# Optimization experiments

Hardware: AMD Instinct MI355X
Metric: run time of the kernel (lower is better)

Reference implementation:

```python
import jax, jax.numpy as jnp
import numpy as np

B, H, W, C = 64, 56, 56, 256
WS, SHIFT, HEADS = 7, 3, 8
N = WS * WS
HID = 4 * C


def _rel_pos_index():
    coords = np.stack(np.meshgrid(np.arange(WS), np.arange(WS), indexing='ij'))  # (2,ws,ws)
    flat = coords.reshape(2, -1)
    rel = (flat[:, :, None] - flat[:, None, :]).transpose(1, 2, 0)  # (N,N,2)
    rel[..., 0] += WS - 1
    rel[..., 1] += WS - 1
    rel[..., 0] *= 2 * WS - 1
    return rel.sum(-1)  # (N,N)


def _attn_mask():
    img = np.zeros((H, W), dtype=np.int32)
    cnt = 0
    for hs in (slice(0, -WS), slice(-WS, -SHIFT), slice(-SHIFT, None)):
        for ws_ in (slice(0, -WS), slice(-WS, -SHIFT), slice(-SHIFT, None)):
            img[hs, ws_] = cnt
            cnt += 1
    mw = img.reshape(H // WS, WS, W // WS, WS).transpose(0, 2, 1, 3).reshape(-1, N)  # (nW,N)
    diff = mw[:, None, :] - mw[:, :, None]
    return np.where(diff != 0, -100.0, 0.0).astype(np.float32)  # (nW,N,N)


def setup_inputs() -> dict:
    key = jax.random.key(0)
    ks = jax.random.split(key, 16)
    s = 0.02
    return {
        'x': jax.random.normal(ks[0], (B, H * W, C), jnp.float32),
        'norm1_g': jnp.ones((C,), jnp.float32),
        'norm1_b': jnp.zeros((C,), jnp.float32),
        'qkv_w': jax.random.normal(ks[1], (3 * C, C), jnp.float32) * s,
        'qkv_b': jnp.zeros((3 * C,), jnp.float32),
        'rpb_table': jax.random.normal(ks[2], ((2 * WS - 1) ** 2, HEADS), jnp.float32) * s,
        'proj_w': jax.random.normal(ks[3], (C, C), jnp.float32) * s,
        'proj_b': jnp.zeros((C,), jnp.float32),
        'norm2_g': jnp.ones((C,), jnp.float32),
        'norm2_b': jnp.zeros((C,), jnp.float32),
        'fc1_w': jax.random.normal(ks[4], (HID, C), jnp.float32) * s,
        'fc1_b': jnp.zeros((HID,), jnp.float32),
        'fc2_w': jax.random.normal(ks[5], (C, HID), jnp.float32) * s,
        'fc2_b': jnp.zeros((C,), jnp.float32),
        'rel_index': jnp.asarray(_rel_pos_index(), jnp.int32),
        'attn_mask': jnp.asarray(_attn_mask(), jnp.float32),
    }


def _ln(y, g, b):
    m = y.mean(-1, keepdims=True)
    v = ((y - m) ** 2).mean(-1, keepdims=True)
    return (y - m) / jnp.sqrt(v + 1e-5) * g + b


def reference(x, norm1_g, norm1_b, qkv_w, qkv_b, rpb_table, proj_w, proj_b,
              norm2_g, norm2_b, fc1_w, fc1_b, fc2_w, fc2_b, rel_index, attn_mask):
    Bx, L, Cx = x.shape
    shortcut = x
    y = _ln(x, norm1_g, norm1_b).reshape(Bx, H, W, Cx)
    # cyclic shift (roll_index_select equivalent)
    y = jnp.roll(y, (-SHIFT, -SHIFT), axis=(1, 2))
    # window partition -> (B*nW, N, C)
    y = y.reshape(Bx, H // WS, WS, W // WS, WS, Cx).transpose(0, 1, 3, 2, 4, 5).reshape(-1, N, Cx)
    B_ = y.shape[0]
    hd = Cx // HEADS
    qkv = (y @ qkv_w.T + qkv_b).reshape(B_, N, 3, HEADS, hd).transpose(2, 0, 3, 1, 4)
    q, k, v = qkv[0], qkv[1], qkv[2]
    scale = hd ** -0.5
    attn = jnp.einsum('bhnd,bhmd->bhnm', q * scale, k)  # (B_,H,N,N)
    rpb = rpb_table[rel_index.reshape(-1)].reshape(N, N, HEADS).transpose(2, 0, 1)
    attn = attn + rpb[None]
    nW = attn_mask.shape[0]
    attn = attn.reshape(B_ // nW, nW, HEADS, N, N) + attn_mask[None, :, None]
    attn = jax.nn.softmax(attn.reshape(B_, HEADS, N, N), axis=-1)
    o = jnp.einsum('bhnm,bhmd->bhnd', attn, v).transpose(0, 2, 1, 3).reshape(B_, N, Cx)
    o = o @ proj_w.T + proj_b
    # window reverse + reverse shift
    o = o.reshape(Bx, H // WS, W // WS, WS, WS, Cx).transpose(0, 1, 3, 2, 4, 5).reshape(Bx, H, W, Cx)
    o = jnp.roll(o, (SHIFT, SHIFT), axis=(1, 2)).reshape(Bx, L, Cx)
    x = shortcut + o  # drop_path prob = 0 / eval mode
    h = _ln(x, norm2_g, norm2_b)
    h = h @ fc1_w.T + fc1_b
    h = h * jax.nn.sigmoid(1.702 * h)  # fast_gelu
    h = h @ fc2_w.T + fc2_b
    return x + h
```

## Files before the change

kernel.cpp:

```cpp
#include <hip/hip_runtime.h>

typedef unsigned short u16;
typedef __attribute__((ext_vector_type(8))) short bf16x8;
typedef __attribute__((ext_vector_type(4))) float f32x4;

struct __align__(8) U16x4 { u16 x, y, z, w; };

__device__ __forceinline__ u16 f2bf(float f) {
  unsigned u = __float_as_uint(f);
  u = (u + 0x7FFFu + ((u >> 16) & 1u)) >> 16;
  return (u16)u;
}

__device__ __forceinline__ void gload16(const u16* g, u16* l) {
  __builtin_amdgcn_global_load_lds((const __attribute__((address_space(1))) void*)g,
                                   (__attribute__((address_space(3))) void*)l, 16, 0, 0);
}

#define MTOK 200704
#define CDIM 256
#define NC3  768
#define HIDD 1024

#define OFF_QKV   0UL
#define OFF_O     308281344UL
#define OFF_H1    0UL
#define OFF_Y     411041792UL
#define OFF_WQ    513802240UL
#define OFF_WP    514195456UL
#define OFF_W1    514326528UL
#define OFF_W2    514850816UL
#define OFF_RPB   515375104UL

__global__ __launch_bounds__(256) void prep_kernel(
    const float* __restrict__ qkv_w, const float* __restrict__ proj_w,
    const float* __restrict__ fc1_w, const float* __restrict__ fc2_w,
    const float* __restrict__ rpb_table, const int* __restrict__ rel_index,
    u16* wq, u16* wp, u16* w1, u16* w2, float* rpbf) {
  int i = blockIdx.x * 256 + threadIdx.x;
  if (i < 196608) { wq[i] = f2bf(qkv_w[i]); return; }
  int j = i - 196608;
  if (j < 65536) { wp[j] = f2bf(proj_w[j]); return; }
  int k = j - 65536;
  if (k < 262144) { w1[k] = f2bf(fc1_w[k]); return; }
  int l = k - 262144;
  if (l < 262144) { w2[l] = f2bf(fc2_w[l]); return; }
  int r = l - 262144;
  if (r < 8 * 2401) {
    int h = r / 2401, nm = r % 2401;
    rpbf[r] = rpb_table[rel_index[nm] * 8 + h];
  }
}

__global__ __launch_bounds__(256) void ln1_kernel(const float* __restrict__ x,
                                                  const float* __restrict__ gg,
                                                  const float* __restrict__ bb,
                                                  u16* __restrict__ y) {
  int wid = threadIdx.x >> 6, lane = threadIdx.x & 63;
  int m = blockIdx.x * 4 + wid;
  int win = m / 49, n = m % 49;
  int b = win >> 6, widx = win & 63;
  int hh = (widx >> 3) * 7 + n / 7 + 3; if (hh >= 56) hh -= 56;
  int ww = (widx & 7) * 7 + n % 7 + 3; if (ww >= 56) ww -= 56;
  const float* src = x + ((size_t)b * 3136 + hh * 56 + ww) * CDIM + lane * 4;
  float4 v = *(const float4*)src;
  float s = v.x + v.y + v.z + v.w;
  float s2 = v.x * v.x + v.y * v.y + v.z * v.z + v.w * v.w;
  for (int o = 32; o; o >>= 1) { s += __shfl_xor(s, o); s2 += __shfl_xor(s2, o); }
  float mean = s * (1.f / 256.f);
  float inv = rsqrtf(s2 * (1.f / 256.f) - mean * mean + 1e-5f);
  int c = lane * 4;
  float4 gv = *(const float4*)(gg + c);
  float4 bv = *(const float4*)(bb + c);
  U16x4 o4;
  o4.x = f2bf((v.x - mean) * inv * gv.x + bv.x);
  o4.y = f2bf((v.y - mean) * inv * gv.y + bv.y);
  o4.z = f2bf((v.z - mean) * inv * gv.z + bv.z);
  o4.w = f2bf((v.w - mean) * inv * gv.w + bv.w);
  *(U16x4*)(y + (size_t)m * CDIM + c) = o4;
}

__global__ __launch_bounds__(256) void ln2_kernel(const float* __restrict__ x2,
                                                  const float* __restrict__ gg,
                                                  const float* __restrict__ bb,
                                                  u16* __restrict__ y) {
  int wid = threadIdx.x >> 6, lane = threadIdx.x & 63;
  int m = blockIdx.x * 4 + wid;
  const float* src = x2 + (size_t)m * CDIM + lane * 4;
  float4 v = *(const float4*)src;
  float s = v.x + v.y + v.z + v.w;
  float s2 = v.x * v.x + v.y * v.y + v.z * v.z + v.w * v.w;
  for (int o = 32; o; o >>= 1) { s += __shfl_xor(s, o); s2 += __shfl_xor(s2, o); }
  float mean = s * (1.f / 256.f);
  float inv = rsqrtf(s2 * (1.f / 256.f) - mean * mean + 1e-5f);
  int c = lane * 4;
  float4 gv = *(const float4*)(gg + c);
  float4 bv = *(const float4*)(bb + c);
  U16x4 o4;
  o4.x = f2bf((v.x - mean) * inv * gv.x + bv.x);
  o4.y = f2bf((v.y - mean) * inv * gv.y + bv.y);
  o4.z = f2bf((v.z - mean) * inv * gv.z + bv.z);
  o4.w = f2bf((v.w - mean) * inv * gv.w + bv.w);
  *(U16x4*)(y + (size_t)m * CDIM + c) = o4;
}

template <int K>
__device__ __forceinline__ void gemm_tile(const u16* __restrict__ A, const u16* __restrict__ B,
                                          int m0, int n0, f32x4 acc[4][4], u16* lds) {
  const int tid = threadIdx.x;
  const int lane = tid & 63;
  const int lr = lane & 15, g = lane >> 4;
  const int wr = (tid >> 6) >> 1, wc = (tid >> 6) & 1;
  const int srow = tid >> 2;
  const int schunk = (tid & 3) ^ ((tid >> 3) & 3);
  const u16* ga = A + (size_t)(m0 + srow) * K + schunk * 8;
  const u16* gb = B + (size_t)(n0 + srow) * K + schunk * 8;
  const int swz = (g ^ ((lr >> 1) & 3)) * 8;

  auto STAGE = [&](int bsel, int k0) {
    u16* la = lds + bsel * 8192 + tid * 8;
    gload16(ga + k0, la);
    gload16(ga + (size_t)64 * K + k0, la + 2048);
    gload16(gb + k0, la + 4096);
    gload16(gb + (size_t)64 * K + k0, la + 6144);
  };
  auto COMPUTE = [&](int bsel) {
    const u16* ba = lds + bsel * 8192;
    const u16* bb = ba + 4096;
    bf16x8 af[4], bfr[4];
#pragma unroll
    for (int i = 0; i < 4; ++i) {
      af[i]  = *(const bf16x8*)(ba + (wr * 64 + i * 16 + lr) * 32 + swz);
      bfr[i] = *(const bf16x8*)(bb + (wc * 64 + i * 16 + lr) * 32 + swz);
    }
#pragma unroll
    for (int i = 0; i < 4; ++i)
#pragma unroll
      for (int j = 0; j < 4; ++j)
        acc[i][j] = __builtin_amdgcn_mfma_f32_16x16x32_bf16(bfr[j], af[i], acc[i][j], 0, 0, 0);
  };

  constexpr int NT = K / 32;
  STAGE(0, 0);
  __syncthreads();
  for (int t = 0; t < NT; t += 2) {
    if (t + 1 < NT) STAGE(1, (t + 1) * 32);
    COMPUTE(0);
    __syncthreads();
    if (t + 2 < NT) STAGE(0, (t + 2) * 32);
    COMPUTE(1);
    __syncthreads();
  }
}

__device__ __forceinline__ int xcd_swz(int bid, int nwg) {
  return (bid & 7) * (nwg >> 3) + (bid >> 3);
}

#define GEMM_PROLOG(NVAL, KVAL)                                            \
  __shared__ u16 lds[16384];                                               \
  const int NTX = (NVAL) / 128;                                            \
  int logical = xcd_swz(blockIdx.x, NTX * (MTOK / 128));                   \
  int m0 = (logical / NTX) * 128, n0 = (logical % NTX) * 128;              \
  f32x4 zero = {0.f, 0.f, 0.f, 0.f};                                       \
  f32x4 acc[4][4] = {{zero, zero, zero, zero}, {zero, zero, zero, zero},   \
                     {zero, zero, zero, zero}, {zero, zero, zero, zero}};  \
  gemm_tile<KVAL>(A, B, m0, n0, acc, lds);                                 \
  const int lane = threadIdx.x & 63;                                       \
  const int lr = lane & 15, g = lane >> 4;                                 \
  const int wid = threadIdx.x >> 6, wr = wid >> 1, wc = wid & 1;

__global__ __launch_bounds__(256) void gemm_qkv(const u16* __restrict__ A, const u16* __restrict__ B,
                                                const float* __restrict__ bias, u16* __restrict__ out) {
  GEMM_PROLOG(NC3, 256)
#pragma unroll
  for (int i = 0; i < 4; ++i) {
    int row = m0 + wr * 64 + i * 16 + lr;
#pragma unroll
    for (int j = 0; j < 4; ++j) {
      int cb = n0 + wc * 64 + j * 16 + g * 4;
      U16x4 o4;
      o4.x = f2bf(acc[i][j][0] + bias[cb + 0]);
      o4.y = f2bf(acc[i][j][1] + bias[cb + 1]);
      o4.z = f2bf(acc[i][j][2] + bias[cb + 2]);
      o4.w = f2bf(acc[i][j][3] + bias[cb + 3]);
      *(U16x4*)(out + (size_t)row * NC3 + cb) = o4;
    }
  }
}

__global__ __launch_bounds__(256) void gemm_proj(const u16* __restrict__ A, const u16* __restrict__ B,
                                                 const float* __restrict__ bias,
                                                 const float* __restrict__ x, float* __restrict__ x2) {
  GEMM_PROLOG(CDIM, 256)
#pragma unroll
  for (int i = 0; i < 4; ++i) {
    int row = m0 + wr * 64 + i * 16 + lr;
    int win = row / 49, n = row % 49;
    int b = win >> 6, widx = win & 63;
    int hh = (widx >> 3) * 7 + n / 7 + 3; if (hh >= 56) hh -= 56;
    int ww = (widx & 7) * 7 + n % 7 + 3; if (ww >= 56) ww -= 56;
    size_t dst = ((size_t)b * 3136 + hh * 56 + ww) * CDIM;
#pragma unroll
    for (int j = 0; j < 4; ++j) {
      int cb = n0 + wc * 64 + j * 16 + g * 4;
      float4 xv = *(const float4*)(x + dst + cb);
      float4 bv = *(const float4*)(bias + cb);
      float4 o4;
      o4.x = xv.x + acc[i][j][0] + bv.x;
      o4.y = xv.y + acc[i][j][1] + bv.y;
      o4.z = xv.z + acc[i][j][2] + bv.z;
      o4.w = xv.w + acc[i][j][3] + bv.w;
      *(float4*)(x2 + dst + cb) = o4;
    }
  }
}

__global__ __launch_bounds__(256) void gemm_fc1(const u16* __restrict__ A, const u16* __restrict__ B,
                                                const float* __restrict__ bias, u16* __restrict__ out) {
  GEMM_PROLOG(HIDD, 256)
#pragma unroll
  for (int i = 0; i < 4; ++i) {
    int row = m0 + wr * 64 + i * 16 + lr;
#pragma unroll
    for (int j = 0; j < 4; ++j) {
      int cb = n0 + wc * 64 + j * 16 + g * 4;
      float4 bv = *(const float4*)(bias + cb);
      float v0 = acc[i][j][0] + bv.x, v1 = acc[i][j][1] + bv.y;
      float v2 = acc[i][j][2] + bv.z, v3 = acc[i][j][3] + bv.w;
      v0 = v0 / (1.f + __expf(-1.702f * v0));
      v1 = v1 / (1.f + __expf(-1.702f * v1));
      v2 = v2 / (1.f + __expf(-1.702f * v2));
      v3 = v3 / (1.f + __expf(-1.702f * v3));
      U16x4 o4 = {f2bf(v0), f2bf(v1), f2bf(v2), f2bf(v3)};
      *(U16x4*)(out + (size_t)row * HIDD + cb) = o4;
    }
  }
}

__global__ __launch_bounds__(256) void gemm_fc2(const u16* __restrict__ A, const u16* __restrict__ B,
                                                const float* __restrict__ bias, float* __restrict__ out) {
  GEMM_PROLOG(CDIM, 1024)
#pragma unroll
  for (int i = 0; i < 4; ++i) {
    int row = m0 + wr * 64 + i * 16 + lr;
#pragma unroll
    for (int j = 0; j < 4; ++j) {
      int cb = n0 + wc * 64 + j * 16 + g * 4;
      float* p = out + (size_t)row * CDIM + cb;
      float4 ov = *(const float4*)p;
      float4 bv = *(const float4*)(bias + cb);
      ov.x += acc[i][j][0] + bv.x;
      ov.y += acc[i][j][1] + bv.y;
      ov.z += acc[i][j][2] + bv.z;
      ov.w += acc[i][j][3] + bv.w;
      *(float4*)p = ov;
    }
  }
}

__global__ __launch_bounds__(256) void attn_kernel(const u16* __restrict__ qkv,
                                                   const float* __restrict__ rpbf,
                                                   const float* __restrict__ mask,
                                                   u16* __restrict__ o) {
  __shared__ u16 p_lds[4][64][72];
  const int lane = threadIdx.x & 63, wid = threadIdx.x >> 6;
  const int lr = lane & 15, g = lane >> 4;
  const int win = blockIdx.x >> 1;
  const int head = (blockIdx.x & 1) * 4 + wid;
  const int widx = win & 63;
  const size_t base = (size_t)win * 49 * NC3 + head * 32;

  bf16x8 aq[4], bk[4];
#pragma unroll
  for (int R = 0; R < 4; ++R) {
    int n = R * 16 + lr; if (n > 48) n = 48;
    aq[R] = *(const bf16x8*)(qkv + base + (size_t)n * NC3 + 8 * g);
  }
#pragma unroll
  for (int Cc = 0; Cc < 4; ++Cc) {
    int mi = Cc * 16 + lr; if (mi > 48) mi = 48;
    bk[Cc] = *(const bf16x8*)(qkv + base + 256 + (size_t)mi * NC3 + 8 * g);
  }
  f32x4 zero = {0.f, 0.f, 0.f, 0.f};
  f32x4 s[4][4] = {{zero, zero, zero, zero}, {zero, zero, zero, zero},
                   {zero, zero, zero, zero}, {zero, zero, zero, zero}};
#pragma unroll
  for (int R = 0; R < 4; ++R)
#pragma unroll
    for (int Cc = 0; Cc < 4; ++Cc)
      s[R][Cc] = __builtin_amdgcn_mfma_f32_16x16x32_bf16(bk[Cc], aq[R], s[R][Cc], 0, 0, 0);

  const float scale = 0.17677669529663687f;
  const float* rpb_h = rpbf + head * 2401;
  const float* msk = mask + widx * 2401;
#pragma unroll
  for (int R = 0; R < 4; ++R) {
    int n = R * 16 + lr;
    bool nok = n < 49;
    int rbase = n * 49;
    float mx = -1e30f;
#pragma unroll
    for (int Cc = 0; Cc < 4; ++Cc)
#pragma unroll
      for (int reg = 0; reg < 4; ++reg) {
        int mc = Cc * 16 + g * 4 + reg;
        float v = (nok && mc < 49)
                    ? s[R][Cc][reg] * scale + rpb_h[rbase + mc] + msk[rbase + mc]
                    : -1e30f;
        s[R][Cc][reg] = v;
        mx = fmaxf(mx, v);
      }
    mx = fmaxf(mx, __shfl_xor(mx, 16));
    mx = fmaxf(mx, __shfl_xor(mx, 32));
    float sum = 0.f;
#pragma unroll
    for (int Cc = 0; Cc < 4; ++Cc)
#pragma unroll
      for (int reg = 0; reg < 4; ++reg) {
        float p = __expf(s[R][Cc][reg] - mx);
        s[R][Cc][reg] = p;
        sum += p;
      }
    sum += __shfl_xor(sum, 16);
    sum += __shfl_xor(sum, 32);
    float rs = 1.f / sum;
    int rowi = R * 16 + lr;
#pragma unroll
    for (int Cc = 0; Cc < 4; ++Cc) {
      U16x4 p4 = {f2bf(s[R][Cc][0] * rs), f2bf(s[R][Cc][1] * rs),
                  f2bf(s[R][Cc][2] * rs), f2bf(s[R][Cc][3] * rs)};
      *(U16x4*)(&p_lds[wid][rowi][Cc * 16 + g * 4]) = p4;
    }
  }
  __syncthreads();

  f32x4 oacc[4][2] = {{zero, zero}, {zero, zero}, {zero, zero}, {zero, zero}};
  const u16* vbase = qkv + base + 512;
#pragma unroll
  for (int ks = 0; ks < 2; ++ks) {
    bf16x8 bv[2];
#pragma unroll
    for (int D = 0; D < 2; ++D) {
#pragma unroll
      for (int i = 0; i < 8; ++i) {
        int mi = ks * 32 + 8 * g + i; if (mi > 48) mi = 48;
        bv[D][i] = (short)vbase[(size_t)mi * NC3 + D * 16 + lr];
      }
    }
#pragma unroll
    for (int R = 0; R < 4; ++R) {
      bf16x8 ap = *(const bf16x8*)(&p_lds[wid][R * 16 + lr][ks * 32 + 8 * g]);
      oacc[R][0] = __builtin_amdgcn_mfma_f32_16x16x32_bf16(bv[0], ap, oacc[R][0], 0, 0, 0);
      oacc[R][1] = __builtin_amdgcn_mfma_f32_16x16x32_bf16(bv[1], ap, oacc[R][1], 0, 0, 0);
    }
  }
#pragma unroll
  for (int R = 0; R < 4; ++R) {
    int n = R * 16 + lr;
    if (n < 49) {
#pragma unroll
      for (int D = 0; D < 2; ++D) {
        U16x4 o4 = {f2bf(oacc[R][D][0]), f2bf(oacc[R][D][1]),
                    f2bf(oacc[R][D][2]), f2bf(oacc[R][D][3])};
        *(U16x4*)(o + ((size_t)win * 49 + n) * CDIM + head * 32 + D * 16 + g * 4) = o4;
      }
    }
  }
}

extern "C" void kernel_launch(void* const* d_in, const int* in_sizes, int n_in,
                              void* d_out, int out_size, void* d_ws, size_t ws_size,
                              hipStream_t stream) {
  const float* x      = (const float*)d_in[0];
  const float* n1g    = (const float*)d_in[1];
  const float* n1b    = (const float*)d_in[2];
  const float* qkv_w  = (const float*)d_in[3];
  const float* qkv_b  = (const float*)d_in[4];
  const float* rpb_t  = (const float*)d_in[5];
  const float* proj_w = (const float*)d_in[6];
  const float* proj_b = (const float*)d_in[7];
  const float* n2g    = (const float*)d_in[8];
  const float* n2b    = (const float*)d_in[9];
  const float* fc1_w  = (const float*)d_in[10];
  const float* fc1_b  = (const float*)d_in[11];
  const float* fc2_w  = (const float*)d_in[12];
  const float* fc2_b  = (const float*)d_in[13];
  const int*   relidx = (const int*)d_in[14];
  const float* amask  = (const float*)d_in[15];
  float* out = (float*)d_out;
  char* ws = (char*)d_ws;

  u16* qkv_buf = (u16*)(ws + OFF_QKV);
  u16* o_buf   = (u16*)(ws + OFF_O);
  u16* h1_buf  = (u16*)(ws + OFF_H1);
  u16* y_buf   = (u16*)(ws + OFF_Y);
  u16* wq = (u16*)(ws + OFF_WQ);
  u16* wp = (u16*)(ws + OFF_WP);
  u16* w1 = (u16*)(ws + OFF_W1);
  u16* w2 = (u16*)(ws + OFF_W2);
  float* rpbf = (float*)(ws + OFF_RPB);

  prep_kernel<<<3148, 256, 0, stream>>>(qkv_w, proj_w, fc1_w, fc2_w, rpb_t, relidx, wq, wp, w1, w2, rpbf);
  ln1_kernel<<<MTOK / 4, 256, 0, stream>>>(x, n1g, n1b, y_buf);
  gemm_qkv<<<(NC3 / 128) * (MTOK / 128), 256, 0, stream>>>(y_buf, wq, qkv_b, qkv_buf);
  attn_kernel<<<4096 * 2, 256, 0, stream>>>(qkv_buf, rpbf, amask, o_buf);
  gemm_proj<<<(CDIM / 128) * (MTOK / 128), 256, 0, stream>>>(o_buf, wp, proj_b, x, out);
  ln2_kernel<<<MTOK / 4, 256, 0, stream>>>(out, n2g, n2b, y_buf);
  gemm_fc1<<<(HIDD / 128) * (MTOK / 128), 256, 0, stream>>>(y_buf, w1, fc1_b, h1_buf);
  gemm_fc2<<<(CDIM / 128) * (MTOK / 128), 256, 0, stream>>>(h1_buf, w2, fc2_b, out);
}
```

Baseline: 1.352 ms.

## Triple-buffer GEMM LDS staging with vmcnt waits and a single barrier per step

Reworks the GEMM main loop from a double buffer with two __syncthreads per pair of k-steps into a three-stage LDS ring. Each step waits on vmcnt so only the oldest async global-to-LDS load must finish, issues one barrier, then prefetches two steps ahead. The aim is to hide global load latency better and cut barrier stalls. It raises LDS use per block from 32 KB to 48 KB, which may lower occupancy, and also swaps the manual bf16 rounding for the HIP intrinsic.

```diff
diff --git a/kernel.cpp b/kernel.cpp
--- a/kernel.cpp
+++ b/kernel.cpp
@@ -1,4 +1,5 @@
 #include <hip/hip_runtime.h>
+#include <hip/hip_bf16.h>
 
 typedef unsigned short u16;
 typedef __attribute__((ext_vector_type(8))) short bf16x8;
@@ -7,9 +8,10 @@
 struct __align__(8) U16x4 { u16 x, y, z, w; };
 
 __device__ __forceinline__ u16 f2bf(float f) {
-  unsigned u = __float_as_uint(f);
-  u = (u + 0x7FFFu + ((u >> 16) & 1u)) >> 16;
-  return (u16)u;
+  __hip_bfloat16 h = __float2bfloat16(f);
+  u16 r;
+  __builtin_memcpy(&r, &h, 2);
+  return r;
 }
 
 __device__ __forceinline__ void gload16(const u16* g, u16* l) {
@@ -116,6 +118,8 @@
   const u16* ga = A + (size_t)(m0 + srow) * K + schunk * 8;
   const u16* gb = B + (size_t)(n0 + srow) * K + schunk * 8;
   const int swz = (g ^ ((lr >> 1) & 3)) * 8;
+  const int aoff = (wr * 64 + lr) * 32 + swz;
+  const int boff = (wc * 64 + lr) * 32 + swz;
 
   auto STAGE = [&](int bsel, int k0) {
     u16* la = lds + bsel * 8192 + tid * 8;
@@ -124,32 +128,30 @@
     gload16(gb + k0, la + 4096);
     gload16(gb + (size_t)64 * K + k0, la + 6144);
   };
-  auto COMPUTE = [&](int bsel) {
-    const u16* ba = lds + bsel * 8192;
+
+  constexpr int NT = K / 32;
+  STAGE(0, 0);
+  STAGE(1, 32);
+#pragma unroll
+  for (int t = 0; t < NT; ++t) {
+    if (t < NT - 1) asm volatile("s_waitcnt vmcnt(4)" ::: "memory");
+    else            asm volatile("s_waitcnt vmcnt(0)" ::: "memory");
+    __builtin_amdgcn_s_barrier();
+    __builtin_amdgcn_sched_barrier(0);
+    if (t < NT - 2) STAGE((t + 2) % 3, (t + 2) * 32);
+    const u16* ba = lds + (t % 3) * 8192;
     const u16* bb = ba + 4096;
     bf16x8 af[4], bfr[4];
 #pragma unroll
     for (int i = 0; i < 4; ++i) {
-      af[i]  = *(const bf16x8*)(ba + (wr * 64 + i * 16 + lr) * 32 + swz);
-      bfr[i] = *(const bf16x8*)(bb + (wc * 64 + i * 16 + lr) * 32 + swz);
+      af[i]  = *(const bf16x8*)(ba + aoff + i * 512);
+      bfr[i] = *(const bf16x8*)(bb + boff + i * 512);
     }
 #pragma unroll
     for (int i = 0; i < 4; ++i)
 #pragma unroll
       for (int j = 0; j < 4; ++j)
         acc[i][j] = __builtin_amdgcn_mfma_f32_16x16x32_bf16(bfr[j], af[i], acc[i][j], 0, 0, 0);
-  };
-
-  constexpr int NT = K / 32;
-  STAGE(0, 0);
-  __syncthreads();
-  for (int t = 0; t < NT; t += 2) {
-    if (t + 1 < NT) STAGE(1, (t + 1) * 32);
-    COMPUTE(0);
-    __syncthreads();
-    if (t + 2 < NT) STAGE(0, (t + 2) * 32);
-    COMPUTE(1);
-    __syncthreads();
   }
 }
 
@@ -158,7 +160,7 @@
 }
 
 #define GEMM_PROLOG(NVAL, KVAL)                                            \
-  __shared__ u16 lds[16384];                                               \
+  __shared__ u16 lds[24576];                                               \
   const int NTX = (NVAL) / 128;                                            \
   int logical = xcd_swz(blockIdx.x, NTX * (MTOK / 128));                   \
   int m0 = (logical / NTX) * 128, n0 = (logical % NTX) * 128;              \
```

Result: no change. 1.343 ms (-0.6%).
